# Performance work log

Measured on AMD Instinct MI355X. Metric: run time of the kernel, lower is better.

## Reference

```python
import jax, jax.numpy as jnp
import numpy as np
from jax import lax

T, B, N_IN, H, N_OUT = 2048, 64, 128, 256, 128

def setup_inputs() -> dict:
    key = jax.random.key(0)
    ks = jax.random.split(key, 7)
    s_ih = 1.0 / np.sqrt(H)
    return {
        "x": jax.random.normal(ks[0], (T, B, N_IN), jnp.float32),
        "w_ih": jax.random.uniform(ks[1], (H, N_IN), jnp.float32, -s_ih, s_ih),
        "w_hh": jax.random.uniform(ks[2], (H, H), jnp.float32, -s_ih, s_ih),
        "b_ih": jax.random.uniform(ks[3], (H,), jnp.float32, -s_ih, s_ih),
        "b_hh": jax.random.uniform(ks[4], (H,), jnp.float32, -s_ih, s_ih),
        "w_out": jax.random.uniform(ks[5], (N_OUT, H), jnp.float32, -1.0/np.sqrt(H), 1.0/np.sqrt(H)),
        "b_out": jax.random.uniform(ks[6], (N_OUT,), jnp.float32, -1.0/np.sqrt(H), 1.0/np.sqrt(H)),
    }

def reference(x, w_ih, w_hh, b_ih, b_hh, w_out, b_out):
    # Vanilla RNN (basic_rnn_step): h_t = tanh(x_t W_ih^T + b_ih + h_{t-1} W_hh^T + b_hh)
    # Precompute input projections for all timesteps in one big GEMM.
    x_proj = jnp.einsum('tbi,hi->tbh', x, w_ih) + b_ih + b_hh  # [T,B,H]

    def step(h, xp_t):
        h = jnp.tanh(xp_t + h @ w_hh.T)
        return h, h

    h0 = jnp.zeros((x.shape[1], w_hh.shape[0]), x.dtype)
    _, hs = lax.scan(step, h0, x_proj)          # hs: [T,B,H]
    # Linear output layer applied at every timestep (has_fc_out -> logits)
    return jnp.einsum('tbh,oh->tbo', hs, w_out) + b_out
```

## Files before the change

kernel.cpp:

```cpp
#include <hip/hip_runtime.h>
#include <hip/hip_bf16.h>
#include <hip/hip_fp16.h>

#define T_ 2048
#define B_ 64
#define NIN_ 128
#define H_ 256
#define NOUT_ 128
#define TB_ (T_*B_)
#define BH_ (B_*H_)
#define TBLK_ (T_/8)

typedef _Float16 h8 __attribute__((ext_vector_type(8)));
typedef _Float16 h4 __attribute__((ext_vector_type(4)));
typedef float f32x4 __attribute__((ext_vector_type(4)));

#define BAR_LGKM() asm volatile("s_waitcnt lgkmcnt(0)\n\ts_barrier" ::: "memory")

__device__ __forceinline__ h8 cvt8(float4 a, float4 b) {
    h8 r;
    r[0] = (_Float16)a.x; r[1] = (_Float16)a.y; r[2] = (_Float16)a.z; r[3] = (_Float16)a.w;
    r[4] = (_Float16)b.x; r[5] = (_Float16)b.y; r[6] = (_Float16)b.z; r[7] = (_Float16)b.w;
    return r;
}
__device__ __forceinline__ h8 ld_cvt8(const float* __restrict__ p) {
    const float4* q = (const float4*)p;
    return cvt8(q[0], q[1]);
}

__global__ __launch_bounds__(256, 2) void k1_xproj(
    const float* __restrict__ x,
    const float* __restrict__ w_ih,
    const float* __restrict__ b_ih,
    const float* __restrict__ b_hh,
    _Float16* __restrict__ xp2)
{
    const int tid = threadIdx.x;
    const int lane = tid & 63, wave = tid >> 6;
    const int m = lane & 15, quad = lane >> 4;
    const int b  = blockIdx.x >> 4;
    const int tc = blockIdx.x & 15;

    h8 af[4][4];
    #pragma unroll
    for (int i = 0; i < 4; ++i)
        #pragma unroll
        for (int kt = 0; kt < 4; ++kt)
            af[i][kt] = ld_cvt8(w_ih + (size_t)(wave*64 + i*16 + m) * NIN_ + kt*32 + quad*8);

    float bias[4][4];
    #pragma unroll
    for (int i = 0; i < 4; ++i)
        #pragma unroll
        for (int r = 0; r < 4; ++r) {
            int c = wave*64 + i*16 + quad*4 + r;
            bias[i][r] = b_ih[c] + b_hh[c];
        }

    __shared__ __align__(16) _Float16 st2[2][256 * 24];

    float4 xr[4][2];
    {
        const int t0 = tc * 128;
        #pragma unroll
        for (int kt = 0; kt < 4; ++kt) {
            const float4* q = (const float4*)(x + ((size_t)(t0 + m) * B_ + b) * NIN_ + kt*32 + quad*8);
            xr[kt][0] = q[0]; xr[kt][1] = q[1];
        }
    }

    for (int rt = 0; rt < 8; ++rt) {
        const int t0 = tc * 128 + rt * 16;

        h8 bf[4];
        #pragma unroll
        for (int kt = 0; kt < 4; ++kt) bf[kt] = cvt8(xr[kt][0], xr[kt][1]);

        if (rt < 7) {
            #pragma unroll
            for (int kt = 0; kt < 4; ++kt) {
                const float4* q = (const float4*)(x + ((size_t)(t0 + 16 + m) * B_ + b) * NIN_ + kt*32 + quad*8);
                xr[kt][0] = q[0]; xr[kt][1] = q[1];
            }
        }

        f32x4 acc[4];
        #pragma unroll
        for (int i = 0; i < 4; ++i) acc[i] = (f32x4){0,0,0,0};
        #pragma unroll
        for (int i = 0; i < 4; ++i)
            #pragma unroll
            for (int kt = 0; kt < 4; ++kt)
                acc[i] = __builtin_amdgcn_mfma_f32_16x16x32_f16(af[i][kt], bf[kt], acc[i], 0, 0, 0);

        const int p = rt & 1;
        #pragma unroll
        for (int i = 0; i < 4; ++i)
            #pragma unroll
            for (int r = 0; r < 4; ++r) {
                int j = wave*64 + i*16 + quad*4 + r;
                st2[p][j*24 + m] = (_Float16)(acc[i][r] + bias[i][r]);
            }
        BAR_LGKM();
        {
            const int j = tid;
            const h8* row = (const h8*)&st2[p][j*24];
            h8 v0 = row[0], v1 = row[1];
            const int blk = t0 >> 3;
            _Float16* dst = xp2 + ((size_t)(b * TBLK_ + blk) * H_ + j) * 8;
            *(h8*)dst            = v0;
            *(h8*)(dst + H_*8)   = v1;
        }
    }
}

__global__ __launch_bounds__(512, 1) void k2_scan(
    const _Float16* __restrict__ xp2,
    const float* __restrict__ w_hh,
    _Float16* __restrict__ hs)
{
    const int tid = threadIdx.x;
    const int lane = tid & 63, wave = tid >> 6;
    const int n = lane & 15, quad = lane >> 4;
    const int b = blockIdx.x;
    const int tsel = quad & 1;
    const int j = wave*32 + tsel*16 + n;
    const bool writer = (quad < 2);

    h8 bf[2][8];
    #pragma unroll
    for (int t = 0; t < 2; ++t)
        #pragma unroll
        for (int kt = 0; kt < 8; ++kt)
            bf[t][kt] = ld_cvt8(w_hh + (size_t)(wave*32 + t*16 + n) * H_ + kt*32 + quad*8);

    __shared__ __align__(16) _Float16 hb[2][256];
    if (tid < 256) hb[0][tid] = (_Float16)0.0f;
    __syncthreads();

    const _Float16* xq = xp2 + ((size_t)b * TBLK_ * H_ + j) * 8;
    _Float16*       hsl = hs + (size_t)b * H_ + j;

    h8 pf = *(const h8*)xq;

#define K2_STEP(T, RB, WB, XV)                                                 \
    {                                                                          \
        const h8* hp = (const h8*)&RB[0];                                      \
        h8 av[8];                                                              \
        _Pragma("unroll")                                                      \
        for (int kt = 0; kt < 8; ++kt) av[kt] = hp[kt*4 + quad];               \
        f32x4 acc[2];                                                          \
        _Pragma("unroll")                                                      \
        for (int t = 0; t < 2; ++t) acc[t] = (f32x4){0,0,0,0};                 \
        _Pragma("unroll")                                                      \
        for (int kt = 0; kt < 8; ++kt)                                         \
            _Pragma("unroll")                                                  \
            for (int t = 0; t < 2; ++t)                                        \
                acc[t] = __builtin_amdgcn_mfma_f32_16x16x32_f16(av[kt], bf[t][kt], acc[t], 0, 0, 0); \
        float vv = tsel ? acc[1][0] : acc[0][0];                               \
        float sv = vv + (XV);                                                  \
        float e  = __expf(2.0f * sv);                                          \
        float hn = fmaf(-2.0f, __builtin_amdgcn_rcpf(e + 1.0f), 1.0f);         \
        _Float16 h16 = (_Float16)hn;                                           \
        if (writer) {                                                          \
            WB[j] = h16;                                                       \
            hsl[(size_t)(T) * BH_] = h16;                                      \
        }                                                                      \
        BAR_LGKM();                                                            \
    }

    for (int tb = 0; tb < TBLK_; ++tb) {
        h8 cur = pf;
        const int tnb = (tb + 1 < TBLK_) ? tb + 1 : TBLK_ - 1;
        pf = *(const h8*)(xq + (size_t)tnb * (H_ * 8));
        const int t = tb * 8;
        K2_STEP(t + 0, hb[0], hb[1], (float)cur[0])
        K2_STEP(t + 1, hb[1], hb[0], (float)cur[1])
        K2_STEP(t + 2, hb[0], hb[1], (float)cur[2])
        K2_STEP(t + 3, hb[1], hb[0], (float)cur[3])
        K2_STEP(t + 4, hb[0], hb[1], (float)cur[4])
        K2_STEP(t + 5, hb[1], hb[0], (float)cur[5])
        K2_STEP(t + 6, hb[0], hb[1], (float)cur[6])
        K2_STEP(t + 7, hb[1], hb[0], (float)cur[7])
    }
#undef K2_STEP
}

__global__ __launch_bounds__(256, 2) void k3_out(
    const _Float16* __restrict__ hs,
    const float* __restrict__ w_out,
    const float* __restrict__ b_out,
    float* __restrict__ out)
{
    const int tid = threadIdx.x;
    const int lane = tid & 63, wave = tid >> 6;
    const int m = lane & 15, quad = lane >> 4;

    h8 af[2][8];
    #pragma unroll
    for (int i = 0; i < 2; ++i)
        #pragma unroll
        for (int kt = 0; kt < 8; ++kt)
            af[i][kt] = ld_cvt8(w_out + (size_t)(wave*32 + i*16 + m) * H_ + kt*32 + quad*8);

    float bias[2][4];
    #pragma unroll
    for (int i = 0; i < 2; ++i)
        #pragma unroll
        for (int r = 0; r < 4; ++r)
            bias[i][r] = b_out[wave*32 + i*16 + quad*4 + r];

    __shared__ __align__(16) float st[2][16][132];

    h8 bf[8];
    {
        const size_t n0 = (size_t)blockIdx.x * 128;
        #pragma unroll
        for (int kt = 0; kt < 8; ++kt)
            bf[kt] = *(const h8*)(hs + (n0 + m) * H_ + kt*32 + quad*8);
    }

    for (int rt = 0; rt < 8; ++rt) {
        const size_t n0 = (size_t)blockIdx.x * 128 + rt * 16;

        h8 cur[8];
        #pragma unroll
        for (int kt = 0; kt < 8; ++kt) cur[kt] = bf[kt];

        if (rt < 7) {
            #pragma unroll
            for (int kt = 0; kt < 8; ++kt)
                bf[kt] = *(const h8*)(hs + (n0 + 16 + m) * H_ + kt*32 + quad*8);
        }

        f32x4 acc[2];
        #pragma unroll
        for (int i = 0; i < 2; ++i) acc[i] = (f32x4){0,0,0,0};
        #pragma unroll
        for (int i = 0; i < 2; ++i)
            #pragma unroll
            for (int kt = 0; kt < 8; ++kt)
                acc[i] = __builtin_amdgcn_mfma_f32_16x16x32_f16(af[i][kt], cur[kt], acc[i], 0, 0, 0);

        const int p = rt & 1;
        #pragma unroll
        for (int i = 0; i < 2; ++i) {
            f32x4 v;
            #pragma unroll
            for (int r = 0; r < 4; ++r) v[r] = acc[i][r] + bias[i][r];
            *(f32x4*)&st[p][m][wave*32 + i*16 + quad*4] = v;
        }
        BAR_LGKM();
        #pragma unroll
        for (int it = 0; it < 2; ++it) {
            int idx = tid + it*256;
            int r = idx >> 5, c4 = (idx & 31) * 4;
            f32x4 v = *(const f32x4*)&st[p][r][c4];
            *(f32x4*)(out + (n0 + r) * NOUT_ + c4) = v;
        }
    }
}

extern "C" void kernel_launch(void* const* d_in, const int* in_sizes, int n_in,
                              void* d_out, int out_size, void* d_ws, size_t ws_size,
                              hipStream_t stream) {
    const float* x     = (const float*)d_in[0];
    const float* w_ih  = (const float*)d_in[1];
    const float* w_hh  = (const float*)d_in[2];
    const float* b_ih  = (const float*)d_in[3];
    const float* b_hh  = (const float*)d_in[4];
    const float* w_out = (const float*)d_in[5];
    const float* b_out = (const float*)d_in[6];

    _Float16* xp2   = (_Float16*)d_ws;
    _Float16* hsbuf = xp2 + (size_t)TB_ * H_;

    k1_xproj<<<1024, 256, 0, stream>>>(x, w_ih, b_ih, b_hh, xp2);
    k2_scan <<<B_,   512, 0, stream>>>(xp2, w_hh, hsbuf);
    k3_out  <<<1024, 256, 0, stream>>>(hsbuf, w_out, b_out, (float*)d_out);
}
```

Measured before the change: 1.018 ms.

## Split recurrent matvec between MFMA and packed-FP16 VALU dot products

In the serial scan step, the 8 K-chunks of the h·W_hh product were all computed with MFMA. Now 5 chunks stay on MFMA and the last 3 are done with packed half2 FMAs on the vector ALU, followed by cross-lane shuffle reductions. The goal is to shorten the per-timestep critical path by running the two units in parallel. The cost is extra shuffles, and accumulating in fp16 reduces precision.

```diff
diff --git a/kernel.cpp b/kernel.cpp
--- a/kernel.cpp
+++ b/kernel.cpp
@@ -13,9 +13,12 @@
 
 typedef _Float16 h8 __attribute__((ext_vector_type(8)));
 typedef _Float16 h4 __attribute__((ext_vector_type(4)));
+typedef _Float16 h2 __attribute__((ext_vector_type(2)));
 typedef float f32x4 __attribute__((ext_vector_type(4)));
 
 #define BAR_LGKM() asm volatile("s_waitcnt lgkmcnt(0)\n\ts_barrier" ::: "memory")
+
+#define PK2(v,p) __builtin_shufflevector((v), (v), 2*(p), 2*(p)+1)
 
 __device__ __forceinline__ h8 cvt8(float4 a, float4 b) {
     h8 r;
@@ -127,12 +130,19 @@
     const int j = wave*32 + tsel*16 + n;
     const bool writer = (quad < 2);
 
-    h8 bf[2][8];
+    h8 bf[2][5];
     #pragma unroll
     for (int t = 0; t < 2; ++t)
         #pragma unroll
-        for (int kt = 0; kt < 8; ++kt)
+        for (int kt = 0; kt < 5; ++kt)
             bf[t][kt] = ld_cvt8(w_hh + (size_t)(wave*32 + t*16 + n) * H_ + kt*32 + quad*8);
+
+    h8 wA[3], wB[3];
+    #pragma unroll
+    for (int c = 0; c < 3; ++c) {
+        wA[c] = ld_cvt8(w_hh + (size_t)(wave*32 + n)      * H_ + (5+c)*32 + quad*8);
+        wB[c] = ld_cvt8(w_hh + (size_t)(wave*32 + 16 + n) * H_ + (5+c)*32 + quad*8);
+    }
 
     __shared__ __align__(16) _Float16 hb[2][256];
     if (tid < 256) hb[0][tid] = (_Float16)0.0f;
@@ -150,15 +160,34 @@
         _Pragma("unroll")                                                      \
         for (int kt = 0; kt < 8; ++kt) av[kt] = hp[kt*4 + quad];               \
         f32x4 acc[2];                                                          \
+        acc[0] = (f32x4){0,0,0,0}; acc[1] = (f32x4){0,0,0,0};                  \
         _Pragma("unroll")                                                      \
-        for (int t = 0; t < 2; ++t) acc[t] = (f32x4){0,0,0,0};                 \
+        for (int kt = 0; kt < 5; ++kt) {                                       \
+            acc[0] = __builtin_amdgcn_mfma_f32_16x16x32_f16(av[kt], bf[0][kt], acc[0], 0, 0, 0); \
+            acc[1] = __builtin_amdgcn_mfma_f32_16x16x32_f16(av[kt], bf[1][kt], acc[1], 0, 0, 0); \
+        }                                                                      \
+        h2 aA0 = (h2){0,0}, aA1 = (h2){0,0}, aB0 = (h2){0,0}, aB1 = (h2){0,0}; \
         _Pragma("unroll")                                                      \
-        for (int kt = 0; kt < 8; ++kt)                                         \
-            _Pragma("unroll")                                                  \
-            for (int t = 0; t < 2; ++t)                                        \
-                acc[t] = __builtin_amdgcn_mfma_f32_16x16x32_f16(av[kt], bf[t][kt], acc[t], 0, 0, 0); \
+        for (int c = 0; c < 3; ++c) {                                          \
+            h8 hv = av[5+c];                                                   \
+            aA0 = PK2(hv,0)*PK2(wA[c],0) + aA0;                                \
+            aA1 = PK2(hv,1)*PK2(wA[c],1) + aA1;                                \
+            aA0 = PK2(hv,2)*PK2(wA[c],2) + aA0;                                \
+            aA1 = PK2(hv,3)*PK2(wA[c],3) + aA1;                                \
+            aB0 = PK2(hv,0)*PK2(wB[c],0) + aB0;                                \
+            aB1 = PK2(hv,1)*PK2(wB[c],1) + aB1;                                \
+            aB0 = PK2(hv,2)*PK2(wB[c],2) + aB0;                                \
+            aB1 = PK2(hv,3)*PK2(wB[c],3) + aB1;                                \
+        }                                                                      \
+        float pA = ((float)aA0[0] + (float)aA0[1]) + ((float)aA1[0] + (float)aA1[1]); \
+        float pB = ((float)aB0[0] + (float)aB0[1]) + ((float)aB1[0] + (float)aB1[1]); \
+        pA += __shfl_xor(pA, 16, 64);                                          \
+        pA += __shfl_xor(pA, 32, 64);                                          \
+        pB += __shfl_xor(pB, 16, 64);                                          \
+        pB += __shfl_xor(pB, 32, 64);                                          \
         float vv = tsel ? acc[1][0] : acc[0][0];                               \
-        float sv = vv + (XV);                                                  \
+        float vt = tsel ? pB : pA;                                             \
+        float sv = vv + vt + (XV);                                             \
         float e  = __expf(2.0f * sv);                                          \
         float hn = fmaf(-2.0f, __builtin_amdgcn_rcpf(e + 1.0f), 1.0f);         \
         _Float16 h16 = (_Float16)hn;                                           \
```

Measured after the change: 1.149 ms. 12.8% more time.

## Fuse input projection into recurrent scan kernel with interleaved MFMA

Applied to the files above, without the earlier changes.

Removes the separate x-projection kernel and computes the input projection for the next 16-step block inside the scan kernel. The loads, the MFMAs and the LDS writes are interleaved between the latency-bound recurrent steps and double-buffered in shared memory. This is meant to drop the launch and the round trip of the large fp16 xp buffer through global memory by using the scan kernel's idle MFMA and memory slots. The risk is extra register pressure and longer steps on the serial critical path of the 64-block scan.

```diff
diff --git a/kernel.cpp b/kernel.cpp
--- a/kernel.cpp
+++ b/kernel.cpp
@@ -9,7 +9,7 @@
 #define NOUT_ 128
 #define TB_ (T_*B_)
 #define BH_ (B_*H_)
-#define TBLK_ (T_/8)
+#define TBLK2_ (T_/16)
 
 typedef _Float16 h8 __attribute__((ext_vector_type(8)));
 typedef _Float16 h4 __attribute__((ext_vector_type(4)));
@@ -28,95 +28,12 @@
     return cvt8(q[0], q[1]);
 }
 
-__global__ __launch_bounds__(256, 2) void k1_xproj(
+__global__ __launch_bounds__(512, 1) void k2_scan(
     const float* __restrict__ x,
     const float* __restrict__ w_ih,
+    const float* __restrict__ w_hh,
     const float* __restrict__ b_ih,
     const float* __restrict__ b_hh,
-    _Float16* __restrict__ xp2)
-{
-    const int tid = threadIdx.x;
-    const int lane = tid & 63, wave = tid >> 6;
-    const int m = lane & 15, quad = lane >> 4;
-    const int b  = blockIdx.x >> 4;
-    const int tc = blockIdx.x & 15;
-
-    h8 af[4][4];
-    #pragma unroll
-    for (int i = 0; i < 4; ++i)
-        #pragma unroll
-        for (int kt = 0; kt < 4; ++kt)
-            af[i][kt] = ld_cvt8(w_ih + (size_t)(wave*64 + i*16 + m) * NIN_ + kt*32 + quad*8);
-
-    float bias[4][4];
-    #pragma unroll
-    for (int i = 0; i < 4; ++i)
-        #pragma unroll
-        for (int r = 0; r < 4; ++r) {
-            int c = wave*64 + i*16 + quad*4 + r;
-            bias[i][r] = b_ih[c] + b_hh[c];
-        }
-
-    __shared__ __align__(16) _Float16 st2[2][256 * 24];
-
-    float4 xr[4][2];
-    {
-        const int t0 = tc * 128;
-        #pragma unroll
-        for (int kt = 0; kt < 4; ++kt) {
-            const float4* q = (const float4*)(x + ((size_t)(t0 + m) * B_ + b) * NIN_ + kt*32 + quad*8);
-            xr[kt][0] = q[0]; xr[kt][1] = q[1];
-        }
-    }
-
-    for (int rt = 0; rt < 8; ++rt) {
-        const int t0 = tc * 128 + rt * 16;
-
-        h8 bf[4];
-        #pragma unroll
-        for (int kt = 0; kt < 4; ++kt) bf[kt] = cvt8(xr[kt][0], xr[kt][1]);
-
-        if (rt < 7) {
-            #pragma unroll
-            for (int kt = 0; kt < 4; ++kt) {
-                const float4* q = (const float4*)(x + ((size_t)(t0 + 16 + m) * B_ + b) * NIN_ + kt*32 + quad*8);
-                xr[kt][0] = q[0]; xr[kt][1] = q[1];
-            }
-        }
-
-        f32x4 acc[4];
-        #pragma unroll
-        for (int i = 0; i < 4; ++i) acc[i] = (f32x4){0,0,0,0};
-        #pragma unroll
-        for (int i = 0; i < 4; ++i)
-            #pragma unroll
-            for (int kt = 0; kt < 4; ++kt)
-                acc[i] = __builtin_amdgcn_mfma_f32_16x16x32_f16(af[i][kt], bf[kt], acc[i], 0, 0, 0);
-
-        const int p = rt & 1;
-        #pragma unroll
-        for (int i = 0; i < 4; ++i)
-            #pragma unroll
-            for (int r = 0; r < 4; ++r) {
-                int j = wave*64 + i*16 + quad*4 + r;
-                st2[p][j*24 + m] = (_Float16)(acc[i][r] + bias[i][r]);
-            }
-        BAR_LGKM();
-        {
-            const int j = tid;
-            const h8* row = (const h8*)&st2[p][j*24];
-            h8 v0 = row[0], v1 = row[1];
-            const int blk = t0 >> 3;
-            _Float16* dst = xp2 + ((size_t)(b * TBLK_ + blk) * H_ + j) * 8;
-            *(h8*)dst            = v0;
-            *(h8*)(dst + H_*8)   = v1;
-        }
-    }
-}
-
-__global__ __launch_bounds__(512, 1) void k2_scan(
-    const _Float16* __restrict__ xp2,
-    const float* __restrict__ w_hh,
     _Float16* __restrict__ hs)
 {
     const int tid = threadIdx.x;
@@ -134,14 +51,68 @@
         for (int kt = 0; kt < 8; ++kt)
             bf[t][kt] = ld_cvt8(w_hh + (size_t)(wave*32 + t*16 + n) * H_ + kt*32 + quad*8);
 
+    h8 bih[2][4];
+    #pragma unroll
+    for (int t = 0; t < 2; ++t)
+        #pragma unroll
+        for (int kt = 0; kt < 4; ++kt)
+            bih[t][kt] = ld_cvt8(w_ih + (size_t)(wave*32 + t*16 + n) * NIN_ + kt*32 + quad*8);
+
+    float xbias[2];
+    #pragma unroll
+    for (int t = 0; t < 2; ++t) {
+        int c = wave*32 + t*16 + n;
+        xbias[t] = b_ih[c] + b_hh[c];
+    }
+
     __shared__ __align__(16) _Float16 hb[2][256];
+    __shared__ __align__(16) _Float16 xpb[2][256][24];
+
+#define LOAD_X(blk)                                                            \
+    {                                                                          \
+        _Pragma("unroll")                                                      \
+        for (int kt = 0; kt < 4; ++kt) {                                       \
+            const float4* q = (const float4*)(x + ((size_t)((blk)*16 + n) * B_ + b) * NIN_ + kt*32 + quad*8); \
+            xr[kt][0] = q[0]; xr[kt][1] = q[1];                                \
+        }                                                                      \
+    }
+
+#define XPROJ_MFMA()                                                           \
+    {                                                                          \
+        xacc[0] = (f32x4){0,0,0,0}; xacc[1] = (f32x4){0,0,0,0};                \
+        _Pragma("unroll")                                                      \
+        for (int kt = 0; kt < 4; ++kt) {                                       \
+            xacc[0] = __builtin_amdgcn_mfma_f32_16x16x32_f16(axv[kt], bih[0][kt], xacc[0], 0, 0, 0); \
+            xacc[1] = __builtin_amdgcn_mfma_f32_16x16x32_f16(axv[kt], bih[1][kt], xacc[1], 0, 0, 0); \
+        }                                                                      \
+    }
+
+#define XPROJ_WRITE(buf)                                                       \
+    {                                                                          \
+        _Pragma("unroll")                                                      \
+        for (int t = 0; t < 2; ++t) {                                          \
+            int c = wave*32 + t*16 + n;                                        \
+            h4 v;                                                              \
+            _Pragma("unroll")                                                  \
+            for (int r = 0; r < 4; ++r) v[r] = (_Float16)(xacc[t][r] + xbias[t]); \
+            *(h4*)&xpb[buf][c][quad*4] = v;                                    \
+        }                                                                      \
+    }
+
+    float4 xr[4][2];
+    h8 axv[4];
+    f32x4 xacc[2];
+
+    LOAD_X(0);
+    #pragma unroll
+    for (int kt = 0; kt < 4; ++kt) axv[kt] = cvt8(xr[kt][0], xr[kt][1]);
+    XPROJ_MFMA();
+    XPROJ_WRITE(0);
+    LOAD_X(1);
     if (tid < 256) hb[0][tid] = (_Float16)0.0f;
     __syncthreads();
 
-    const _Float16* xq = xp2 + ((size_t)b * TBLK_ * H_ + j) * 8;
-    _Float16*       hsl = hs + (size_t)b * H_ + j;
-
-    h8 pf = *(const h8*)xq;
+    _Float16* hsl = hs + (size_t)b * H_ + j;
 
 #define K2_STEP(T, RB, WB, XV)                                                 \
     {                                                                          \
@@ -150,13 +121,12 @@
         _Pragma("unroll")                                                      \
         for (int kt = 0; kt < 8; ++kt) av[kt] = hp[kt*4 + quad];               \
         f32x4 acc[2];                                                          \
-        _Pragma("unroll")                                                      \
-        for (int t = 0; t < 2; ++t) acc[t] = (f32x4){0,0,0,0};                 \
-        _Pragma("unroll")                                                      \
-        for (int kt = 0; kt < 8; ++kt)                                         \
-            _Pragma("unroll")                                                  \
-            for (int t = 0; t < 2; ++t)                                        \
-                acc[t] = __builtin_amdgcn_mfma_f32_16x16x32_f16(av[kt], bf[t][kt], acc[t], 0, 0, 0); \
+        acc[0] = (f32x4){0,0,0,0}; acc[1] = (f32x4){0,0,0,0};                  \
+        _Pragma("unroll")                                                      \
+        for (int kt = 0; kt < 8; ++kt) {                                       \
+            acc[0] = __builtin_amdgcn_mfma_f32_16x16x32_f16(av[kt], bf[0][kt], acc[0], 0, 0, 0); \
+            acc[1] = __builtin_amdgcn_mfma_f32_16x16x32_f16(av[kt], bf[1][kt], acc[1], 0, 0, 0); \
+        }                                                                      \
         float vv = tsel ? acc[1][0] : acc[0][0];                               \
         float sv = vv + (XV);                                                  \
         float e  = __expf(2.0f * sv);                                          \
@@ -169,21 +139,41 @@
         BAR_LGKM();                                                            \
     }
 
-    for (int tb = 0; tb < TBLK_; ++tb) {
-        h8 cur = pf;
-        const int tnb = (tb + 1 < TBLK_) ? tb + 1 : TBLK_ - 1;
-        pf = *(const h8*)(xq + (size_t)tnb * (H_ * 8));
-        const int t = tb * 8;
-        K2_STEP(t + 0, hb[0], hb[1], (float)cur[0])
-        K2_STEP(t + 1, hb[1], hb[0], (float)cur[1])
-        K2_STEP(t + 2, hb[0], hb[1], (float)cur[2])
-        K2_STEP(t + 3, hb[1], hb[0], (float)cur[3])
-        K2_STEP(t + 4, hb[0], hb[1], (float)cur[4])
-        K2_STEP(t + 5, hb[1], hb[0], (float)cur[5])
-        K2_STEP(t + 6, hb[0], hb[1], (float)cur[6])
-        K2_STEP(t + 7, hb[1], hb[0], (float)cur[7])
+    for (int tb = 0; tb < TBLK2_; ++tb) {
+        const int p = tb & 1;
+        const int t0 = tb * 16;
+        const bool gen = (tb < TBLK2_ - 1);
+
+        h8 cur0 = *(const h8*)&xpb[p][j][0];
+        K2_STEP(t0 + 0, hb[0], hb[1], (float)cur0[0])
+        if (gen) {
+            #pragma unroll
+            for (int kt = 0; kt < 4; ++kt) axv[kt] = cvt8(xr[kt][0], xr[kt][1]);
+        }
+        K2_STEP(t0 + 1, hb[1], hb[0], (float)cur0[1])
+        if (gen) { XPROJ_MFMA(); }
+        K2_STEP(t0 + 2, hb[0], hb[1], (float)cur0[2])
+        if (gen) { XPROJ_WRITE(p ^ 1); }
+        K2_STEP(t0 + 3, hb[1], hb[0], (float)cur0[3])
+        if (tb < TBLK2_ - 2) { LOAD_X(tb + 2); }
+        K2_STEP(t0 + 4, hb[0], hb[1], (float)cur0[4])
+        K2_STEP(t0 + 5, hb[1], hb[0], (float)cur0[5])
+        K2_STEP(t0 + 6, hb[0], hb[1], (float)cur0[6])
+        K2_STEP(t0 + 7, hb[1], hb[0], (float)cur0[7])
+        h8 cur1 = *(const h8*)&xpb[p][j][8];
+        K2_STEP(t0 + 8,  hb[0], hb[1], (float)cur1[0])
+        K2_STEP(t0 + 9,  hb[1], hb[0], (float)cur1[1])
+        K2_STEP(t0 + 10, hb[0], hb[1], (float)cur1[2])
+        K2_STEP(t0 + 11, hb[1], hb[0], (float)cur1[3])
+        K2_STEP(t0 + 12, hb[0], hb[1], (float)cur1[4])
+        K2_STEP(t0 + 13, hb[1], hb[0], (float)cur1[5])
+        K2_STEP(t0 + 14, hb[0], hb[1], (float)cur1[6])
+        K2_STEP(t0 + 15, hb[1], hb[0], (float)cur1[7])
     }
 #undef K2_STEP
+#undef LOAD_X
+#undef XPROJ_MFMA
+#undef XPROJ_WRITE
 }
 
 __global__ __launch_bounds__(256, 2) void k3_out(
@@ -272,10 +262,8 @@
     const float* w_out = (const float*)d_in[5];
     const float* b_out = (const float*)d_in[6];
 
-    _Float16* xp2   = (_Float16*)d_ws;
-    _Float16* hsbuf = xp2 + (size_t)TB_ * H_;
-
-    k1_xproj<<<1024, 256, 0, stream>>>(x, w_ih, b_ih, b_hh, xp2);
-    k2_scan <<<B_,   512, 0, stream>>>(xp2, w_hh, hsbuf);
-    k3_out  <<<1024, 256, 0, stream>>>(hsbuf, w_out, b_out, (float*)d_out);
-}
+    _Float16* hsbuf = (_Float16*)d_ws;
+
+    k2_scan<<<B_,   512, 0, stream>>>(x, w_ih, w_hh, b_ih, b_hh, hsbuf);
+    k3_out <<<1024, 256, 0, stream>>>(hsbuf, w_out, b_out, (float*)d_out);
+}
```

After: 1.056 ms. 1.04x slower.
